# Optimization experiments

Measured on AMD Instinct MI355X. Metric: run time of the kernel, lower is better.

The kernel has to match this reference:

```python
import jax, jax.numpy as jnp
import numpy as np

B, REP = 32, 1024
N_VERBS, N_ROLES, N_NOUNS, MR = 504, 190, 11538, 6
HID, NHEADS, MAXN = 32, 4, 512


def setup_inputs() -> dict:
    key = jax.random.key(0)
    ks = jax.random.split(key, 16)
    s = 0.05  # weight scale
    return {
        "rep": jax.random.normal(ks[0], (B, REP), jnp.float32),
        "W_v": jax.random.normal(ks[1], (REP, N_VERBS), jnp.float32) * s,
        "b_v": jax.random.normal(ks[2], (N_VERBS,), jnp.float32) * s,
        "W_r": jax.random.normal(ks[3], (REP, N_ROLES * HID), jnp.float32) * s,
        "b_r": jax.random.normal(ks[4], (N_ROLES * HID,), jnp.float32) * s,
        "attn_in_w": jax.random.normal(ks[5], (3, 3 * HID, HID), jnp.float32) * s,
        "attn_in_b": jax.random.normal(ks[6], (3, 3 * HID), jnp.float32) * s,
        "attn_out_w": jax.random.normal(ks[7], (3, HID, HID), jnp.float32) * s,
        "attn_out_b": jax.random.normal(ks[8], (3, HID), jnp.float32) * s,
        "W_n": jax.random.normal(ks[9], (HID, N_NOUNS), jnp.float32) * s,
        "b_n": jax.random.normal(ks[10], (N_NOUNS,), jnp.float32) * s,
        "r_n_idx": jax.random.randint(ks[11], (N_ROLES, MAXN), 0, N_NOUNS, jnp.int32),
        "pad_v_r": jax.random.randint(ks[12], (N_VERBS, MR), 0, N_ROLES + 1, jnp.int32),
    }


def _mha(x, in_w, in_b, out_w, out_b):
    # x: [L, B, E] self-attention, torch nn.MultiheadAttention semantics
    L, Bn, E = x.shape
    hd = E // NHEADS
    qkv = x @ in_w.T + in_b                      # [L, B, 3E]
    q, k, v = jnp.split(qkv, 3, axis=-1)
    q = q.reshape(L, Bn, NHEADS, hd)
    k = k.reshape(L, Bn, NHEADS, hd)
    v = v.reshape(L, Bn, NHEADS, hd)
    scores = jnp.einsum("lbhd,mbhd->bhlm", q, k) / jnp.sqrt(jnp.float32(hd))
    attn = jax.nn.softmax(scores, axis=-1)
    out = jnp.einsum("bhlm,mbhd->lbhd", attn, v).reshape(L, Bn, E)
    return out @ out_w.T + out_b


def reference(rep, W_v, b_v, W_r, b_r, attn_in_w, attn_in_b, attn_out_w,
              attn_out_b, W_n, b_n, r_n_idx, pad_v_r):
    batch = rep.shape[0]
    v_potential = rep @ W_v + b_v                          # [B, V]
    node = (rep @ W_r + b_r).reshape(batch, N_ROLES, HID)
    node = jnp.transpose(node, (1, 0, 2))                  # [R, B, H]
    for i in range(3):
        node = _mha(node, attn_in_w[i], attn_in_b[i], attn_out_w[i], attn_out_b[i])
    rn_potential = node @ W_n + b_n                        # [R, B, N_nouns]

    # grouped index_select per role: [R, B, MAXN]
    grouped = jax.vmap(lambda pot, idx: pot[:, idx])(rn_potential, r_n_idx)
    r_max = grouped.max(axis=-1)                           # [R, B]
    maxi = grouped.argmax(axis=-1)                         # [R, B]
    rn_marginal = r_max + jnp.log(jnp.exp(grouped - r_max[..., None]).sum(-1))
    r_maxi = jax.vmap(lambda idx, mi: idx[mi])(r_n_idx, maxi)  # global noun ids

    # [B, R] then prepend the zero/padding column -> [B, 1+R]
    zeros_f = jnp.zeros((batch, 1), rn_marginal.dtype)
    zeros_i = jnp.zeros((batch, 1), r_maxi.dtype)
    rn_marginal = jnp.concatenate([zeros_f, rn_marginal.T], axis=1)
    r_max = jnp.concatenate([zeros_f, r_max.T], axis=1)
    r_maxi = jnp.concatenate([zeros_i, r_maxi.T], axis=1)

    # gather per-verb role groups: [B, V, MR]
    vrn_marginal_g = rn_marginal[:, pad_v_r]
    vr_max_g = r_max[:, pad_v_r]
    vr_maxi_g = r_maxi[:, pad_v_r]

    v_marginal = vrn_marginal_g.sum(2) + v_potential       # [B, V]
    m = v_marginal.max(1)
    norm = m + jnp.log(jnp.exp(v_marginal - m[:, None]).sum(1))
    v_max = vr_max_g.sum(2) + v_potential                  # [B, V]
    return (rep, v_potential, rn_potential, norm, v_max, vr_maxi_g)
```

## Files before the change

### kernel.cpp

```cpp
#include <hip/hip_runtime.h>
#include <math.h>

#define B_    32
#define REP_  1024
#define NV_   504
#define NR_   190
#define NN_   11538
#define MR_   6
#define HID_  32
#define NH_   4
#define HD_   8
#define MAXN_ 512

#define O_VP   32768
#define O_RN   48896
#define O_NORM 70199936
#define O_VMAX 70199968
#define O_MAXI 70216096

#define W_REPT  0
#define W_WT    32768
#define W_PN    401984
#define W_PV    1958464
#define W_N0    2087488
#define W_N1    2282048
#define W_HO    2476608
#define W_MARG  2671168
#define W_RMAX  2677248
#define W_RMAXI 2683328

__global__ __launch_bounds__(256) void k_tr_rep(const float* __restrict__ rep,
                                                float* __restrict__ repT) {
    int gid = blockIdx.x * 256 + threadIdx.x;
    int b = gid & 31, k = gid >> 5;
    repT[gid] = rep[b * REP_ + k];
}

__global__ __launch_bounds__(256) void k_tr_wn(const float* __restrict__ Wn,
                                               float* __restrict__ Wt) {
    __shared__ float t[32][33];
    int n0 = blockIdx.x * 32;
    int tid = threadIdx.x;
    #pragma unroll
    for (int p = 0; p < 4; p++) {
        int idx = p * 256 + tid;
        int k = idx >> 5, n = idx & 31;
        int nn = n0 + n;
        t[k][n] = (nn < NN_) ? Wn[(size_t)k * NN_ + nn] : 0.f;
    }
    __syncthreads();
    #pragma unroll
    for (int p = 0; p < 4; p++) {
        int idx = p * 256 + tid;
        int n = idx >> 5, k = idx & 31;
        int nn = n0 + n;
        if (nn < NN_) Wt[nn * 32 + k] = t[k][n];
    }
}

__global__ __launch_bounds__(256) void k_gemm_node(const float* __restrict__ Wr,
                                                   const float4* __restrict__ repT4,
                                                   float* __restrict__ pn) {
    int c  = blockIdx.x * 64 + (threadIdx.x & 63);
    int bg = threadIdx.x >> 6;
    int k0 = blockIdx.y * 128;
    float acc[8] = {0.f,0.f,0.f,0.f,0.f,0.f,0.f,0.f};
    int rbase = k0 * 8 + bg * 2;
    const float* w = Wr + (size_t)k0 * 6080 + c;
    #pragma unroll 4
    for (int k = 0; k < 128; k++) {
        float wv = w[(size_t)k * 6080];
        float4 ra = repT4[rbase + k * 8];
        float4 rb = repT4[rbase + k * 8 + 1];
        acc[0] += ra.x * wv; acc[1] += ra.y * wv; acc[2] += ra.z * wv; acc[3] += ra.w * wv;
        acc[4] += rb.x * wv; acc[5] += rb.y * wv; acc[6] += rb.z * wv; acc[7] += rb.w * wv;
    }
    size_t base = (size_t)blockIdx.y * 194560 + (size_t)(bg * 8) * 6080 + c;
    #pragma unroll
    for (int i = 0; i < 8; i++) pn[base + (size_t)i * 6080] = acc[i];
}

__global__ __launch_bounds__(256) void k_gemm_vp(const float* __restrict__ Wv,
                                                 const float4* __restrict__ repT4,
                                                 float* __restrict__ pv) {
    int c  = blockIdx.x * 64 + (threadIdx.x & 63);
    if (c >= NV_) return;
    int bg = threadIdx.x >> 6;
    int k0 = blockIdx.y * 128;
    float acc[8] = {0.f,0.f,0.f,0.f,0.f,0.f,0.f,0.f};
    int rbase = k0 * 8 + bg * 2;
    const float* w = Wv + (size_t)k0 * NV_ + c;
    #pragma unroll 4
    for (int k = 0; k < 128; k++) {
        float wv = w[(size_t)k * NV_];
        float4 ra = repT4[rbase + k * 8];
        float4 rb = repT4[rbase + k * 8 + 1];
        acc[0] += ra.x * wv; acc[1] += ra.y * wv; acc[2] += ra.z * wv; acc[3] += ra.w * wv;
        acc[4] += rb.x * wv; acc[5] += rb.y * wv; acc[6] += rb.z * wv; acc[7] += rb.w * wv;
    }
    size_t base = (size_t)blockIdx.y * 16128 + (size_t)(bg * 8) * NV_ + c;
    #pragma unroll
    for (int i = 0; i < 8; i++) pv[base + (size_t)i * NV_] = acc[i];
}

__global__ __launch_bounds__(256) void k_reduce(const float* __restrict__ pn,
                                                const float* __restrict__ pv,
                                                const float* __restrict__ br,
                                                const float* __restrict__ bv,
                                                float* __restrict__ node0,
                                                float* __restrict__ vpot) {
    int bid = blockIdx.x, tid = threadIdx.x;
    if (bid < 760) {
        int gid = bid * 256 + tid;
        int b = gid / 6080, c = gid - b * 6080;
        float s = br[c];
        #pragma unroll
        for (int kz = 0; kz < 8; kz++) s += pn[kz * 194560 + gid];
        node0[(c >> 5) * 1024 + b * 32 + (c & 31)] = s;
    } else {
        int gid = (bid - 760) * 256 + tid;
        int v = gid % NV_;
        float s = bv[v];
        #pragma unroll
        for (int kz = 0; kz < 8; kz++) s += pv[kz * 16128 + gid];
        vpot[gid] = s;
    }
}

__global__ __launch_bounds__(256) void k_attn(const float* __restrict__ xin,
                                              const float* __restrict__ inw,
                                              const float* __restrict__ inb,
                                              float* __restrict__ ho) {
    int b = blockIdx.x >> 2, h = blockIdx.x & 3;
    int tid = threadIdx.x;
    __shared__ __align__(16) float qs[192 * 12];
    __shared__ __align__(16) float ks[192 * 12];
    __shared__ __align__(16) float vs[192 * 12];
    __shared__ __align__(16) float pmS[4 * 192];
    __shared__ __align__(16) float psS[4 * 192];
    __shared__ __align__(16) float poS[4 * 192 * 8];

    if (tid < NR_) {
        const float* xr = xin + tid * 1024 + b * 32;
        float4 xv[8];
        #pragma unroll
        for (int q = 0; q < 8; q++) xv[q] = *(const float4*)(xr + q * 4);
        #pragma unroll 1
        for (int part = 0; part < 3; part++) {
            float* dst = (part == 0) ? qs : (part == 1) ? ks : vs;
            #pragma unroll 1
            for (int jj = 0; jj < 8; jj++) {
                int row = part * 32 + h * 8 + jj;
                const float* wr = inw + row * 32;
                float s = inb[row];
                #pragma unroll
                for (int q = 0; q < 8; q++) {
                    s += xv[q].x * wr[q*4+0] + xv[q].y * wr[q*4+1] +
                         xv[q].z * wr[q*4+2] + xv[q].w * wr[q*4+3];
                }
                dst[tid * 12 + jj] = s;
            }
        }
    }
    __syncthreads();

    int wave = tid >> 6, lane = tid & 63;
    int m0 = wave * 48;
    int m1 = (m0 + 48 < NR_) ? (m0 + 48) : NR_;
    float4 qa[3], qb[3];
    #pragma unroll
    for (int i = 0; i < 3; i++) {
        int l = lane + 64 * i;
        if (l < NR_) {
            qa[i] = *(const float4*)&qs[l * 12];
            qb[i] = *(const float4*)&qs[l * 12 + 4];
        } else {
            qa[i] = make_float4(0.f,0.f,0.f,0.f);
            qb[i] = make_float4(0.f,0.f,0.f,0.f);
        }
    }
    float mM[3] = {-INFINITY, -INFINITY, -INFINITY};
    float sS[3] = {0.f, 0.f, 0.f};
    float o[3][8];
    #pragma unroll
    for (int i = 0; i < 3; i++)
        #pragma unroll
        for (int d = 0; d < 8; d++) o[i][d] = 0.f;
    const float scale = 0.3535533905932738f;
    for (int mm = m0; mm < m1; mm++) {
        float4 ka = *(const float4*)&ks[mm * 12];
        float4 kb = *(const float4*)&ks[mm * 12 + 4];
        float4 va = *(const float4*)&vs[mm * 12];
        float4 vb = *(const float4*)&vs[mm * 12 + 4];
        #pragma unroll
        for (int i = 0; i < 3; i++) {
            float sc = (qa[i].x*ka.x + qa[i].y*ka.y + qa[i].z*ka.z + qa[i].w*ka.w +
                        qb[i].x*kb.x + qb[i].y*kb.y + qb[i].z*kb.z + qb[i].w*kb.w) * scale;
            if (sc > mM[i]) {
                float al = __expf(mM[i] - sc);
                sS[i] = sS[i] * al + 1.f;
                mM[i] = sc;
                o[i][0] = o[i][0]*al + va.x; o[i][1] = o[i][1]*al + va.y;
                o[i][2] = o[i][2]*al + va.z; o[i][3] = o[i][3]*al + va.w;
                o[i][4] = o[i][4]*al + vb.x; o[i][5] = o[i][5]*al + vb.y;
                o[i][6] = o[i][6]*al + vb.z; o[i][7] = o[i][7]*al + vb.w;
            } else {
                float p = __expf(sc - mM[i]);
                sS[i] += p;
                o[i][0] += p*va.x; o[i][1] += p*va.y; o[i][2] += p*va.z; o[i][3] += p*va.w;
                o[i][4] += p*vb.x; o[i][5] += p*vb.y; o[i][6] += p*vb.z; o[i][7] += p*vb.w;
            }
        }
    }
    #pragma unroll
    for (int i = 0; i < 3; i++) {
        int slot = wave * 192 + lane + 64 * i;
        pmS[slot] = mM[i];
        psS[slot] = sS[i];
        *(float4*)&poS[slot * 8]     = make_float4(o[i][0], o[i][1], o[i][2], o[i][3]);
        *(float4*)&poS[slot * 8 + 4] = make_float4(o[i][4], o[i][5], o[i][6], o[i][7]);
    }
    __syncthreads();

    if (tid < NR_) {
        float M = pmS[tid], S = psS[tid];
        float4 oa = *(const float4*)&poS[tid * 8];
        float4 ob = *(const float4*)&poS[tid * 8 + 4];
        #pragma unroll
        for (int w = 1; w < 4; w++) {
            int slot = w * 192 + tid;
            float m2 = pmS[slot], s2 = psS[slot];
            float4 pa = *(const float4*)&poS[slot * 8];
            float4 pb = *(const float4*)&poS[slot * 8 + 4];
            if (m2 > M) {
                float al = __expf(M - m2);
                S = S * al + s2;
                oa.x = oa.x*al + pa.x; oa.y = oa.y*al + pa.y; oa.z = oa.z*al + pa.z; oa.w = oa.w*al + pa.w;
                ob.x = ob.x*al + pb.x; ob.y = ob.y*al + pb.y; ob.z = ob.z*al + pb.z; ob.w = ob.w*al + pb.w;
                M = m2;
            } else {
                float p = __expf(m2 - M);
                S += s2 * p;
                oa.x += p*pa.x; oa.y += p*pa.y; oa.z += p*pa.z; oa.w += p*pa.w;
                ob.x += p*pb.x; ob.y += p*pb.y; ob.z += p*pb.z; ob.w += p*pb.w;
            }
        }
        float inv = 1.f / S;
        float* hp = ho + tid * 1024 + b * 32 + h * 8;
        *(float4*)hp       = make_float4(oa.x*inv, oa.y*inv, oa.z*inv, oa.w*inv);
        *(float4*)(hp + 4) = make_float4(ob.x*inv, ob.y*inv, ob.z*inv, ob.w*inv);
    }
}

__global__ __launch_bounds__(256) void k_outproj(const float* __restrict__ ho,
                                                 const float* __restrict__ ow,
                                                 const float* __restrict__ ob,
                                                 float* __restrict__ xout) {
    int l = blockIdx.x >> 2, part = blockIdx.x & 3;
    int tid = threadIdx.x;
    __shared__ float w[32 * 33];
    __shared__ float hl[256];
    __shared__ float obs[32];
    for (int i = tid; i < 1024; i += 256) w[(i >> 5) * 33 + (i & 31)] = ow[i];
    if (tid < 32) obs[tid] = ob[tid];
    {
        int bb = tid >> 5, e = tid & 31;
        hl[tid] = ho[l * 1024 + (part * 8 + bb) * 32 + e];
    }
    __syncthreads();
    int bb = tid >> 5, e = tid & 31;
    float s = obs[e];
    #pragma unroll
    for (int e2 = 0; e2 < 32; e2++) s += hl[bb * 32 + e2] * w[e * 33 + e2];
    xout[l * 1024 + (part * 8 + bb) * 32 + e] = s;
}

__global__ __launch_bounds__(256) void k_rnpot(const float* __restrict__ node,
                                               const float* __restrict__ Wn,
                                               const float* __restrict__ bn,
                                               float* __restrict__ out) {
    int tid = threadIdx.x;
    int t0 = blockIdx.x * 32;
    int c0 = blockIdx.y * 512;
    int wave = tid >> 6, lane = tid & 63;
    int r0 = wave * 8;
    int c = c0 + lane * 8;
    __shared__ float As[32 * 32];
    for (int i = tid; i < 1024; i += 256) As[i] = node[t0 * 32 + i];
    __syncthreads();
    int rem = NN_ - c;
    if (rem <= 0) return;
    if (rem >= 8) {
        float acc[8][8];
        #pragma unroll
        for (int r = 0; r < 8; r++)
            #pragma unroll
            for (int q = 0; q < 8; q++) acc[r][q] = 0.f;
        #pragma unroll 1
        for (int g = 0; g < 8; g++) {
            float4 av[8];
            #pragma unroll
            for (int r = 0; r < 8; r++)
                av[r] = *(const float4*)&As[(r0 + r) * 32 + g * 4];
            #pragma unroll
            for (int kk = 0; kk < 4; kk++) {
                int k = g * 4 + kk;
                const float* wp = &Wn[(size_t)k * NN_ + c];
                float2 w0 = *(const float2*)(wp);
                float2 w1 = *(const float2*)(wp + 2);
                float2 w2 = *(const float2*)(wp + 4);
                float2 w3 = *(const float2*)(wp + 6);
                #pragma unroll
                for (int r = 0; r < 8; r++) {
                    float a = ((const float*)&av[r])[kk];
                    acc[r][0] += a * w0.x; acc[r][1] += a * w0.y;
                    acc[r][2] += a * w1.x; acc[r][3] += a * w1.y;
                    acc[r][4] += a * w2.x; acc[r][5] += a * w2.y;
                    acc[r][6] += a * w3.x; acc[r][7] += a * w3.y;
                }
            }
        }
        float bb[8];
        #pragma unroll
        for (int q = 0; q < 8; q++) bb[q] = bn[c + q];
        #pragma unroll
        for (int r = 0; r < 8; r++) {
            size_t base = (size_t)(t0 + r0 + r) * NN_ + c;
            #pragma unroll
            for (int q = 0; q < 4; q++) {
                float2 s = make_float2(acc[r][2*q] + bb[2*q], acc[r][2*q+1] + bb[2*q+1]);
                *(float2*)&out[base + 2*q] = s;
            }
        }
    } else {
        for (int e = 0; e < rem; e++) {
            float acc[8] = {0.f,0.f,0.f,0.f,0.f,0.f,0.f,0.f};
            for (int k = 0; k < 32; k++) {
                float wv = Wn[(size_t)k * NN_ + c + e];
                #pragma unroll
                for (int r = 0; r < 8; r++) acc[r] += As[(r0 + r) * 32 + k] * wv;
            }
            float bv2 = bn[c + e];
            #pragma unroll
            for (int r = 0; r < 8; r++)
                out[(size_t)(t0 + r0 + r) * NN_ + c + e] = acc[r] + bv2;
        }
    }
}

__global__ __launch_bounds__(256) void k_grouped(const float* __restrict__ node,
                                                 const float* __restrict__ Wt,
                                                 const float* __restrict__ bn,
                                                 const int* __restrict__ rni,
                                                 float* __restrict__ marg,
                                                 float* __restrict__ rmax,
                                                 int* __restrict__ rmaxi) {
    int l = blockIdx.x;
    int tid = threadIdx.x;
    int jg = tid >> 5, b = tid & 31;
    __shared__ float pm[32 * 8], psum[32 * 8];
    __shared__ int pj[32 * 8];
    float4 nd[8];
    const float4* np = (const float4*)&node[l * 1024 + b * 32];
    #pragma unroll
    for (int q = 0; q < 8; q++) nd[q] = np[q];
    float lm = -INFINITY, ls = 0.f;
    int jm = 0;
    const int* ip = &rni[l * 512];
    for (int jj = 0; jj < 64; jj++) {
        int j = jg * 64 + jj;
        int idx = ip[j];
        const float4* wr = (const float4*)&Wt[idx * 32];
        float s = bn[idx];
        #pragma unroll
        for (int q = 0; q < 8; q++) {
            float4 w4 = wr[q];
            s += nd[q].x*w4.x + nd[q].y*w4.y + nd[q].z*w4.z + nd[q].w*w4.w;
        }
        if (s > lm) { ls = ls * __expf(lm - s) + 1.f; lm = s; jm = j; }
        else        { ls += __expf(s - lm); }
    }
    pm[b * 8 + jg] = lm; psum[b * 8 + jg] = ls; pj[b * 8 + jg] = jm;
    __syncthreads();
    if (tid < 32) {
        int bb = tid;
        float M = pm[bb * 8], S = psum[bb * 8];
        int J = pj[bb * 8];
        for (int i = 1; i < 8; i++) {
            float m2 = pm[bb * 8 + i], s2 = psum[bb * 8 + i];
            if (m2 > M) { S = S * __expf(M - m2) + s2; M = m2; J = pj[bb * 8 + i]; }
            else        { S += s2 * __expf(m2 - M); }
        }
        int t = l * 32 + bb;
        marg[t]  = M + logf(S);
        rmax[t]  = M;
        rmaxi[t] = ip[J];
    }
}

__global__ __launch_bounds__(256) void k_final(const float* __restrict__ marg,
                                               const float* __restrict__ rmax,
                                               const int* __restrict__ rmaxi,
                                               const int* __restrict__ pad,
                                               const float* __restrict__ vpot,
                                               float* __restrict__ out_norm,
                                               float* __restrict__ out_vmax,
                                               float* __restrict__ out_maxi) {
    int b = blockIdx.x, tid = threadIdx.x;
    __shared__ float me[191], xe[191];
    __shared__ int ie[191];
    __shared__ float vm[NV_];
    __shared__ float rbuf[4];
    if (tid < 191) {
        if (tid == 0) { me[0] = 0.f; xe[0] = 0.f; ie[0] = 0; }
        else {
            int t = (tid - 1) * 32 + b;
            me[tid] = marg[t]; xe[tid] = rmax[t]; ie[tid] = rmaxi[t];
        }
    }
    __syncthreads();
    for (int v = tid; v < NV_; v += 256) {
        float sm = 0.f, sx = 0.f;
        float vp = vpot[b * NV_ + v];
        #pragma unroll
        for (int i = 0; i < 6; i++) {
            int p = pad[v * 6 + i];
            sm += me[p]; sx += xe[p];
            out_maxi[(size_t)(b * NV_ + v) * 6 + i] = (float)ie[p];
        }
        vm[v] = sm + vp;
        out_vmax[b * NV_ + v] = sx + vp;
    }
    __syncthreads();
    float m = -INFINITY;
    for (int v = tid; v < NV_; v += 256) m = fmaxf(m, vm[v]);
    #pragma unroll
    for (int off = 32; off > 0; off >>= 1) m = fmaxf(m, __shfl_xor(m, off));
    if ((tid & 63) == 0) rbuf[tid >> 6] = m;
    __syncthreads();
    float M = fmaxf(fmaxf(rbuf[0], rbuf[1]), fmaxf(rbuf[2], rbuf[3]));
    __syncthreads();
    float s = 0.f;
    for (int v = tid; v < NV_; v += 256) s += __expf(vm[v] - M);
    #pragma unroll
    for (int off = 32; off > 0; off >>= 1) s += __shfl_xor(s, off);
    if ((tid & 63) == 0) rbuf[tid >> 6] = s;
    __syncthreads();
    if (tid == 0) out_norm[b] = M + logf(rbuf[0] + rbuf[1] + rbuf[2] + rbuf[3]);
}

extern "C" void kernel_launch(void* const* d_in, const int* in_sizes, int n_in,
                              void* d_out, int out_size, void* d_ws, size_t ws_size,
                              hipStream_t stream) {
    const float* rep   = (const float*)d_in[0];
    const float* Wv    = (const float*)d_in[1];
    const float* bv    = (const float*)d_in[2];
    const float* Wr    = (const float*)d_in[3];
    const float* br    = (const float*)d_in[4];
    const float* ainw  = (const float*)d_in[5];
    const float* ainb  = (const float*)d_in[6];
    const float* aoutw = (const float*)d_in[7];
    const float* aoutb = (const float*)d_in[8];
    const float* Wn    = (const float*)d_in[9];
    const float* bn    = (const float*)d_in[10];
    const int*   rni   = (const int*)d_in[11];
    const int*   pad   = (const int*)d_in[12];
    float* out = (float*)d_out;
    float* ws  = (float*)d_ws;

    float* repT = ws + W_REPT;
    float* Wt   = ws + W_WT;
    float* pn   = ws + W_PN;
    float* pv   = ws + W_PV;
    float* n0   = ws + W_N0;
    float* n1   = ws + W_N1;
    float* ho   = ws + W_HO;
    float* marg = ws + W_MARG;
    float* rmx  = ws + W_RMAX;
    int*   rmi  = (int*)(ws + W_RMAXI);

    hipMemcpyAsync(out, rep, 32768 * sizeof(float), hipMemcpyDeviceToDevice, stream);
    k_tr_rep<<<128, 256, 0, stream>>>(rep, repT);
    k_tr_wn<<<361, 256, 0, stream>>>(Wn, Wt);
    k_gemm_node<<<dim3(95, 8), 256, 0, stream>>>(Wr, (const float4*)repT, pn);
    k_gemm_vp<<<dim3(8, 8), 256, 0, stream>>>(Wv, (const float4*)repT, pv);
    k_reduce<<<823, 256, 0, stream>>>(pn, pv, br, bv, n0, out + O_VP);

    float* bufs[4] = {n0, n1, n0, n1};
    for (int i = 0; i < 3; i++) {
        k_attn<<<128, 256, 0, stream>>>(bufs[i], ainw + i * 96 * 32, ainb + i * 96, ho);
        k_outproj<<<760, 256, 0, stream>>>(ho, aoutw + i * 32 * 32, aoutb + i * 32, bufs[i + 1]);
    }

    k_rnpot<<<dim3(190, 23), 256, 0, stream>>>(n1, Wn, bn, out + O_RN);
    k_grouped<<<190, 256, 0, stream>>>(n1, Wt, bn, rni, marg, rmx, rmi);
    k_final<<<32, 256, 0, stream>>>(marg, rmx, rmi, pad, out + O_VP,
                                    out + O_NORM, out + O_VMAX, out + O_MAXI);
}
```

Before: 647.0 us.

## Fold attention out-projections into next in-projection and fuse final projection into noun kernels

Precomputes combined weights (in_w[i+1]·out_w[i] and the matching bias) so each attention layer reads the previous layer's head outputs directly, which removes the separate out-projection kernels. The last out-projection is recomputed inside a merged kernel that handles both the role-noun potential GEMM and the grouped logsumexp/argmax, replacing two launches. The two rep GEMMs are merged into one launch, the Wn transpose shares a launch with the weight-combination work, and the rn-potential stores are widened to float4 where aligned. The trade-off is redundant out-projection work repeated in every block and a small change in floating-point rounding order.

```diff
diff --git a/kernel.cpp b/kernel.cpp
--- a/kernel.cpp
+++ b/kernel.cpp
@@ -23,11 +23,12 @@
 #define W_PN    401984
 #define W_PV    1958464
 #define W_N0    2087488
-#define W_N1    2282048
-#define W_HO    2476608
+#define W_HOB   2282048
+#define W_HOA   2476608
 #define W_MARG  2671168
 #define W_RMAX  2677248
 #define W_RMAXI 2683328
+#define W_WC    2689408
 
 __global__ __launch_bounds__(256) void k_tr_rep(const float* __restrict__ rep,
                                                 float* __restrict__ repT) {
@@ -36,71 +37,98 @@
     repT[gid] = rep[b * REP_ + k];
 }
 
-__global__ __launch_bounds__(256) void k_tr_wn(const float* __restrict__ Wn,
-                                               float* __restrict__ Wt) {
+__global__ __launch_bounds__(256) void k_pre(const float* __restrict__ Wn,
+                                             float* __restrict__ Wt,
+                                             const float* __restrict__ ainw,
+                                             const float* __restrict__ ainb,
+                                             const float* __restrict__ aoutw,
+                                             const float* __restrict__ aoutb,
+                                             float* __restrict__ wc) {
     __shared__ float t[32][33];
-    int n0 = blockIdx.x * 32;
     int tid = threadIdx.x;
-    #pragma unroll
-    for (int p = 0; p < 4; p++) {
-        int idx = p * 256 + tid;
-        int k = idx >> 5, n = idx & 31;
-        int nn = n0 + n;
-        t[k][n] = (nn < NN_) ? Wn[(size_t)k * NN_ + nn] : 0.f;
-    }
-    __syncthreads();
-    #pragma unroll
-    for (int p = 0; p < 4; p++) {
-        int idx = p * 256 + tid;
-        int n = idx >> 5, k = idx & 31;
-        int nn = n0 + n;
-        if (nn < NN_) Wt[nn * 32 + k] = t[k][n];
-    }
-}
-
-__global__ __launch_bounds__(256) void k_gemm_node(const float* __restrict__ Wr,
-                                                   const float4* __restrict__ repT4,
-                                                   float* __restrict__ pn) {
-    int c  = blockIdx.x * 64 + (threadIdx.x & 63);
+    if (blockIdx.x < 361) {
+        int n0 = blockIdx.x * 32;
+        #pragma unroll
+        for (int p = 0; p < 4; p++) {
+            int idx = p * 256 + tid;
+            int k = idx >> 5, n = idx & 31;
+            int nn = n0 + n;
+            t[k][n] = (nn < NN_) ? Wn[(size_t)k * NN_ + nn] : 0.f;
+        }
+        __syncthreads();
+        #pragma unroll
+        for (int p = 0; p < 4; p++) {
+            int idx = p * 256 + tid;
+            int n = idx >> 5, k = idx & 31;
+            int nn = n0 + n;
+            if (nn < NN_) Wt[nn * 32 + k] = t[k][n];
+        }
+    } else {
+        #pragma unroll 1
+        for (int layer = 0; layer < 2; layer++) {
+            const float* iw  = ainw + (layer + 1) * 3072;
+            const float* ib  = ainb + (layer + 1) * 96;
+            const float* ow  = aoutw + layer * 1024;
+            const float* obv = aoutb + layer * 32;
+            float* W = wc + layer * 3168;
+            for (int idx = tid; idx < 3072; idx += 256) {
+                int row = idx >> 5, d = idx & 31;
+                float s = 0.f;
+                #pragma unroll
+                for (int e = 0; e < 32; e++) s += iw[row * 32 + e] * ow[e * 32 + d];
+                W[idx] = s;
+            }
+            if (tid < 96) {
+                float s = ib[tid];
+                #pragma unroll
+                for (int e = 0; e < 32; e++) s += iw[tid * 32 + e] * obv[e];
+                W[3072 + tid] = s;
+            }
+        }
+    }
+}
+
+__global__ __launch_bounds__(256) void k_gemm(const float* __restrict__ Wr,
+                                              const float* __restrict__ Wv,
+                                              const float4* __restrict__ repT4,
+                                              float* __restrict__ pn,
+                                              float* __restrict__ pv) {
+    int bx = blockIdx.x;
+    int lane = threadIdx.x & 63;
     int bg = threadIdx.x >> 6;
     int k0 = blockIdx.y * 128;
+    int rbase = k0 * 8 + bg * 2;
     float acc[8] = {0.f,0.f,0.f,0.f,0.f,0.f,0.f,0.f};
-    int rbase = k0 * 8 + bg * 2;
-    const float* w = Wr + (size_t)k0 * 6080 + c;
-    #pragma unroll 4
-    for (int k = 0; k < 128; k++) {
-        float wv = w[(size_t)k * 6080];
-        float4 ra = repT4[rbase + k * 8];
-        float4 rb = repT4[rbase + k * 8 + 1];
-        acc[0] += ra.x * wv; acc[1] += ra.y * wv; acc[2] += ra.z * wv; acc[3] += ra.w * wv;
-        acc[4] += rb.x * wv; acc[5] += rb.y * wv; acc[6] += rb.z * wv; acc[7] += rb.w * wv;
-    }
-    size_t base = (size_t)blockIdx.y * 194560 + (size_t)(bg * 8) * 6080 + c;
-    #pragma unroll
-    for (int i = 0; i < 8; i++) pn[base + (size_t)i * 6080] = acc[i];
-}
-
-__global__ __launch_bounds__(256) void k_gemm_vp(const float* __restrict__ Wv,
-                                                 const float4* __restrict__ repT4,
-                                                 float* __restrict__ pv) {
-    int c  = blockIdx.x * 64 + (threadIdx.x & 63);
-    if (c >= NV_) return;
-    int bg = threadIdx.x >> 6;
-    int k0 = blockIdx.y * 128;
-    float acc[8] = {0.f,0.f,0.f,0.f,0.f,0.f,0.f,0.f};
-    int rbase = k0 * 8 + bg * 2;
-    const float* w = Wv + (size_t)k0 * NV_ + c;
-    #pragma unroll 4
-    for (int k = 0; k < 128; k++) {
-        float wv = w[(size_t)k * NV_];
-        float4 ra = repT4[rbase + k * 8];
-        float4 rb = repT4[rbase + k * 8 + 1];
-        acc[0] += ra.x * wv; acc[1] += ra.y * wv; acc[2] += ra.z * wv; acc[3] += ra.w * wv;
-        acc[4] += rb.x * wv; acc[5] += rb.y * wv; acc[6] += rb.z * wv; acc[7] += rb.w * wv;
-    }
-    size_t base = (size_t)blockIdx.y * 16128 + (size_t)(bg * 8) * NV_ + c;
-    #pragma unroll
-    for (int i = 0; i < 8; i++) pv[base + (size_t)i * NV_] = acc[i];
+    if (bx < 95) {
+        int c = bx * 64 + lane;
+        const float* w = Wr + (size_t)k0 * 6080 + c;
+        #pragma unroll 4
+        for (int k = 0; k < 128; k++) {
+            float wv = w[(size_t)k * 6080];
+            float4 ra = repT4[rbase + k * 8];
+            float4 rb = repT4[rbase + k * 8 + 1];
+            acc[0] += ra.x * wv; acc[1] += ra.y * wv; acc[2] += ra.z * wv; acc[3] += ra.w * wv;
+            acc[4] += rb.x * wv; acc[5] += rb.y * wv; acc[6] += rb.z * wv; acc[7] += rb.w * wv;
+        }
+        size_t base = (size_t)blockIdx.y * 194560 + (size_t)(bg * 8) * 6080 + c;
+        #pragma unroll
+        for (int i = 0; i < 8; i++) pn[base + (size_t)i * 6080] = acc[i];
+    } else {
+        int c = (bx - 95) * 64 + lane;
+        if (c >= NV_) return;
+        const float* w = Wv + (size_t)k0 * NV_ + c;
+        #pragma unroll 4
+        for (int k = 0; k < 128; k++) {
+            float wv = w[(size_t)k * NV_];
+            float4 ra = repT4[rbase + k * 8];
+            float4 rb = repT4[rbase + k * 8 + 1];
+            acc[0] += ra.x * wv; acc[1] += ra.y * wv; acc[2] += ra.z * wv; acc[3] += ra.w * wv;
+            acc[4] += rb.x * wv; acc[5] += rb.y * wv; acc[6] += rb.z * wv; acc[7] += rb.w * wv;
+        }
+        size_t base = (size_t)blockIdx.y * 16128 + (size_t)(bg * 8) * NV_ + c;
+        #pragma unroll
+        for (int i = 0; i < 8; i++) pv[base + (size_t)i * NV_] = acc[i];
+    }
 }
 
 __global__ __launch_bounds__(256) void k_reduce(const float* __restrict__ pn,
@@ -128,8 +156,8 @@
 }
 
 __global__ __launch_bounds__(256) void k_attn(const float* __restrict__ xin,
-                                              const float* __restrict__ inw,
-                                              const float* __restrict__ inb,
+                                              const float* __restrict__ winw,
+                                              const float* __restrict__ winb,
                                               float* __restrict__ ho) {
     int b = blockIdx.x >> 2, h = blockIdx.x & 3;
     int tid = threadIdx.x;
@@ -151,8 +179,8 @@
             #pragma unroll 1
             for (int jj = 0; jj < 8; jj++) {
                 int row = part * 32 + h * 8 + jj;
-                const float* wr = inw + row * 32;
-                float s = inb[row];
+                const float* wr = winw + row * 32;
+                float s = winb[row];
                 #pragma unroll
                 for (int q = 0; q < 8; q++) {
                     s += xv[q].x * wr[q*4+0] + xv[q].y * wr[q*4+1] +
@@ -252,149 +280,185 @@
     }
 }
 
-__global__ __launch_bounds__(256) void k_outproj(const float* __restrict__ ho,
-                                                 const float* __restrict__ ow,
-                                                 const float* __restrict__ ob,
-                                                 float* __restrict__ xout) {
-    int l = blockIdx.x >> 2, part = blockIdx.x & 3;
-    int tid = threadIdx.x;
-    __shared__ float w[32 * 33];
-    __shared__ float hl[256];
-    __shared__ float obs[32];
-    for (int i = tid; i < 1024; i += 256) w[(i >> 5) * 33 + (i & 31)] = ow[i];
-    if (tid < 32) obs[tid] = ob[tid];
-    {
-        int bb = tid >> 5, e = tid & 31;
-        hl[tid] = ho[l * 1024 + (part * 8 + bb) * 32 + e];
-    }
-    __syncthreads();
-    int bb = tid >> 5, e = tid & 31;
-    float s = obs[e];
-    #pragma unroll
-    for (int e2 = 0; e2 < 32; e2++) s += hl[bb * 32 + e2] * w[e * 33 + e2];
-    xout[l * 1024 + (part * 8 + bb) * 32 + e] = s;
-}
-
-__global__ __launch_bounds__(256) void k_rnpot(const float* __restrict__ node,
-                                               const float* __restrict__ Wn,
-                                               const float* __restrict__ bn,
-                                               float* __restrict__ out) {
-    int tid = threadIdx.x;
-    int t0 = blockIdx.x * 32;
-    int c0 = blockIdx.y * 512;
-    int wave = tid >> 6, lane = tid & 63;
-    int r0 = wave * 8;
-    int c = c0 + lane * 8;
-    __shared__ float As[32 * 32];
-    for (int i = tid; i < 1024; i += 256) As[i] = node[t0 * 32 + i];
-    __syncthreads();
-    int rem = NN_ - c;
-    if (rem <= 0) return;
-    if (rem >= 8) {
-        float acc[8][8];
-        #pragma unroll
-        for (int r = 0; r < 8; r++)
-            #pragma unroll
-            for (int q = 0; q < 8; q++) acc[r][q] = 0.f;
-        #pragma unroll 1
-        for (int g = 0; g < 8; g++) {
-            float4 av[8];
-            #pragma unroll
-            for (int r = 0; r < 8; r++)
-                av[r] = *(const float4*)&As[(r0 + r) * 32 + g * 4];
-            #pragma unroll
-            for (int kk = 0; kk < 4; kk++) {
-                int k = g * 4 + kk;
-                const float* wp = &Wn[(size_t)k * NN_ + c];
-                float2 w0 = *(const float2*)(wp);
-                float2 w1 = *(const float2*)(wp + 2);
-                float2 w2 = *(const float2*)(wp + 4);
-                float2 w3 = *(const float2*)(wp + 6);
-                #pragma unroll
-                for (int r = 0; r < 8; r++) {
-                    float a = ((const float*)&av[r])[kk];
-                    acc[r][0] += a * w0.x; acc[r][1] += a * w0.y;
-                    acc[r][2] += a * w1.x; acc[r][3] += a * w1.y;
-                    acc[r][4] += a * w2.x; acc[r][5] += a * w2.y;
-                    acc[r][6] += a * w3.x; acc[r][7] += a * w3.y;
-                }
-            }
-        }
-        float bb[8];
-        #pragma unroll
-        for (int q = 0; q < 8; q++) bb[q] = bn[c + q];
-        #pragma unroll
-        for (int r = 0; r < 8; r++) {
-            size_t base = (size_t)(t0 + r0 + r) * NN_ + c;
-            #pragma unroll
-            for (int q = 0; q < 4; q++) {
-                float2 s = make_float2(acc[r][2*q] + bb[2*q], acc[r][2*q+1] + bb[2*q+1]);
-                *(float2*)&out[base + 2*q] = s;
-            }
-        }
-    } else {
-        for (int e = 0; e < rem; e++) {
-            float acc[8] = {0.f,0.f,0.f,0.f,0.f,0.f,0.f,0.f};
-            for (int k = 0; k < 32; k++) {
-                float wv = Wn[(size_t)k * NN_ + c + e];
-                #pragma unroll
-                for (int r = 0; r < 8; r++) acc[r] += As[(r0 + r) * 32 + k] * wv;
-            }
-            float bv2 = bn[c + e];
-            #pragma unroll
-            for (int r = 0; r < 8; r++)
-                out[(size_t)(t0 + r0 + r) * NN_ + c + e] = acc[r] + bv2;
-        }
-    }
-}
-
-__global__ __launch_bounds__(256) void k_grouped(const float* __restrict__ node,
-                                                 const float* __restrict__ Wt,
-                                                 const float* __restrict__ bn,
-                                                 const int* __restrict__ rni,
-                                                 float* __restrict__ marg,
-                                                 float* __restrict__ rmax,
-                                                 int* __restrict__ rmaxi) {
+__global__ __launch_bounds__(256) void k_big(const float* __restrict__ ho3,
+                                             const float* __restrict__ ow3,
+                                             const float* __restrict__ ob3,
+                                             const float* __restrict__ Wn,
+                                             const float* __restrict__ bn,
+                                             const float* __restrict__ Wt,
+                                             const int* __restrict__ rni,
+                                             float* __restrict__ out_rn,
+                                             float* __restrict__ marg,
+                                             float* __restrict__ rmax,
+                                             int* __restrict__ rmaxi) {
     int l = blockIdx.x;
     int tid = threadIdx.x;
-    int jg = tid >> 5, b = tid & 31;
+    __shared__ float owT[1024];
+    __shared__ float As[1024];
     __shared__ float pm[32 * 8], psum[32 * 8];
-    __shared__ int pj[32 * 8];
-    float4 nd[8];
-    const float4* np = (const float4*)&node[l * 1024 + b * 32];
-    #pragma unroll
-    for (int q = 0; q < 8; q++) nd[q] = np[q];
-    float lm = -INFINITY, ls = 0.f;
-    int jm = 0;
-    const int* ip = &rni[l * 512];
-    for (int jj = 0; jj < 64; jj++) {
-        int j = jg * 64 + jj;
-        int idx = ip[j];
-        const float4* wr = (const float4*)&Wt[idx * 32];
-        float s = bn[idx];
+    __shared__ int   pj[32 * 8];
+
+    for (int i = tid; i < 1024; i += 256) {
+        int d = i >> 5, hh = i & 31;
+        owT[i] = ow3[hh * 32 + d];
+    }
+
+    if (blockIdx.y < 23) {
+        int b = tid >> 3, hq = tid & 7;
+        float4 hv[8];
+        {
+            const float4* hp = (const float4*)&ho3[(size_t)l * 1024 + b * 32];
+            #pragma unroll
+            for (int q = 0; q < 8; q++) hv[q] = hp[q];
+        }
+        __syncthreads();
+        {
+            float4 a = *(const float4*)&ob3[hq * 4];
+            #pragma unroll
+            for (int dq = 0; dq < 8; dq++) {
+                float4 h4 = hv[dq];
+                float4 w0 = *(const float4*)&owT[(dq*4+0)*32 + hq*4];
+                float4 w1 = *(const float4*)&owT[(dq*4+1)*32 + hq*4];
+                float4 w2 = *(const float4*)&owT[(dq*4+2)*32 + hq*4];
+                float4 w3 = *(const float4*)&owT[(dq*4+3)*32 + hq*4];
+                a.x += h4.x*w0.x + h4.y*w1.x + h4.z*w2.x + h4.w*w3.x;
+                a.y += h4.x*w0.y + h4.y*w1.y + h4.z*w2.y + h4.w*w3.y;
+                a.z += h4.x*w0.z + h4.y*w1.z + h4.z*w2.z + h4.w*w3.z;
+                a.w += h4.x*w0.w + h4.y*w1.w + h4.z*w2.w + h4.w*w3.w;
+            }
+            *(float4*)&As[b * 32 + hq * 4] = a;
+        }
+        __syncthreads();
+
+        int t0 = l * 32;
+        int c0 = blockIdx.y * 512;
+        int wave = tid >> 6, lane = tid & 63;
+        int r0 = wave * 8;
+        int c = c0 + lane * 8;
+        int rem = NN_ - c;
+        if (rem <= 0) return;
+        if (rem >= 8) {
+            float acc[8][8];
+            #pragma unroll
+            for (int r = 0; r < 8; r++)
+                #pragma unroll
+                for (int q = 0; q < 8; q++) acc[r][q] = 0.f;
+            #pragma unroll 1
+            for (int g = 0; g < 8; g++) {
+                float4 av[8];
+                #pragma unroll
+                for (int r = 0; r < 8; r++)
+                    av[r] = *(const float4*)&As[(r0 + r) * 32 + g * 4];
+                #pragma unroll
+                for (int kk = 0; kk < 4; kk++) {
+                    int k = g * 4 + kk;
+                    const float* wp = &Wn[(size_t)k * NN_ + c];
+                    float2 w0 = *(const float2*)(wp);
+                    float2 w1 = *(const float2*)(wp + 2);
+                    float2 w2 = *(const float2*)(wp + 4);
+                    float2 w3 = *(const float2*)(wp + 6);
+                    #pragma unroll
+                    for (int r = 0; r < 8; r++) {
+                        float a = ((const float*)&av[r])[kk];
+                        acc[r][0] += a * w0.x; acc[r][1] += a * w0.y;
+                        acc[r][2] += a * w1.x; acc[r][3] += a * w1.y;
+                        acc[r][4] += a * w2.x; acc[r][5] += a * w2.y;
+                        acc[r][6] += a * w3.x; acc[r][7] += a * w3.y;
+                    }
+                }
+            }
+            float bb[8];
+            #pragma unroll
+            for (int q = 0; q < 8; q++) bb[q] = bn[c + q];
+            #pragma unroll
+            for (int r = 0; r < 8; r++) {
+                size_t base = (size_t)(t0 + r0 + r) * NN_ + c;
+                float v0 = acc[r][0]+bb[0], v1 = acc[r][1]+bb[1];
+                float v2 = acc[r][2]+bb[2], v3 = acc[r][3]+bb[3];
+                float v4 = acc[r][4]+bb[4], v5 = acc[r][5]+bb[5];
+                float v6 = acc[r][6]+bb[6], v7 = acc[r][7]+bb[7];
+                if (((r0 + r) & 1) == 0) {
+                    *(float4*)&out_rn[base]     = make_float4(v0, v1, v2, v3);
+                    *(float4*)&out_rn[base + 4] = make_float4(v4, v5, v6, v7);
+                } else {
+                    *(float2*)&out_rn[base]     = make_float2(v0, v1);
+                    *(float4*)&out_rn[base + 2] = make_float4(v2, v3, v4, v5);
+                    *(float2*)&out_rn[base + 6] = make_float2(v6, v7);
+                }
+            }
+        } else {
+            for (int e = 0; e < rem; e++) {
+                float acc[8] = {0.f,0.f,0.f,0.f,0.f,0.f,0.f,0.f};
+                for (int k = 0; k < 32; k++) {
+                    float wv = Wn[(size_t)k * NN_ + c + e];
+                    #pragma unroll
+                    for (int r = 0; r < 8; r++) acc[r] += As[(r0 + r) * 32 + k] * wv;
+                }
+                float bv2 = bn[c + e];
+                #pragma unroll
+                for (int r = 0; r < 8; r++)
+                    out_rn[(size_t)(t0 + r0 + r) * NN_ + c + e] = acc[r] + bv2;
+            }
+        }
+    } else {
+        int jg = tid >> 5, b = tid & 31;
+        float4 hv[8];
+        {
+            const float4* hp = (const float4*)&ho3[(size_t)l * 1024 + b * 32];
+            #pragma unroll
+            for (int q = 0; q < 8; q++) hv[q] = hp[q];
+        }
+        __syncthreads();
+        float4 nd[8];
         #pragma unroll
         for (int q = 0; q < 8; q++) {
-            float4 w4 = wr[q];
-            s += nd[q].x*w4.x + nd[q].y*w4.y + nd[q].z*w4.z + nd[q].w*w4.w;
-        }
-        if (s > lm) { ls = ls * __expf(lm - s) + 1.f; lm = s; jm = j; }
-        else        { ls += __expf(s - lm); }
-    }
-    pm[b * 8 + jg] = lm; psum[b * 8 + jg] = ls; pj[b * 8 + jg] = jm;
-    __syncthreads();
-    if (tid < 32) {
-        int bb = tid;
-        float M = pm[bb * 8], S = psum[bb * 8];
-        int J = pj[bb * 8];
-        for (int i = 1; i < 8; i++) {
-            float m2 = pm[bb * 8 + i], s2 = psum[bb * 8 + i];
-            if (m2 > M) { S = S * __expf(M - m2) + s2; M = m2; J = pj[bb * 8 + i]; }
-            else        { S += s2 * __expf(m2 - M); }
-        }
-        int t = l * 32 + bb;
-        marg[t]  = M + logf(S);
-        rmax[t]  = M;
-        rmaxi[t] = ip[J];
+            float4 a = *(const float4*)&ob3[q * 4];
+            #pragma unroll
+            for (int dq = 0; dq < 8; dq++) {
+                float4 h4 = hv[dq];
+                float4 w0 = *(const float4*)&owT[(dq*4+0)*32 + q*4];
+                float4 w1 = *(const float4*)&owT[(dq*4+1)*32 + q*4];
+                float4 w2 = *(const float4*)&owT[(dq*4+2)*32 + q*4];
+                float4 w3 = *(const float4*)&owT[(dq*4+3)*32 + q*4];
+                a.x += h4.x*w0.x + h4.y*w1.x + h4.z*w2.x + h4.w*w3.x;
+                a.y += h4.x*w0.y + h4.y*w1.y + h4.z*w2.y + h4.w*w3.y;
+                a.z += h4.x*w0.z + h4.y*w1.z + h4.z*w2.z + h4.w*w3.z;
+                a.w += h4.x*w0.w + h4.y*w1.w + h4.z*w2.w + h4.w*w3.w;
+            }
+            nd[q] = a;
+        }
+        float lm = -INFINITY, ls = 0.f;
+        int jm = 0;
+        const int* ip = &rni[l * 512];
+        for (int jj = 0; jj < 64; jj++) {
+            int j = jg * 64 + jj;
+            int idx = ip[j];
+            const float4* wr = (const float4*)&Wt[idx * 32];
+            float s = bn[idx];
+            #pragma unroll
+            for (int q = 0; q < 8; q++) {
+                float4 w4 = wr[q];
+                s += nd[q].x*w4.x + nd[q].y*w4.y + nd[q].z*w4.z + nd[q].w*w4.w;
+            }
+            if (s > lm) { ls = ls * __expf(lm - s) + 1.f; lm = s; jm = j; }
+            else        { ls += __expf(s - lm); }
+        }
+        pm[b * 8 + jg] = lm; psum[b * 8 + jg] = ls; pj[b * 8 + jg] = jm;
+        __syncthreads();
+        if (tid < 32) {
+            int bb = tid;
+            float M = pm[bb * 8], S = psum[bb * 8];
+            int J = pj[bb * 8];
+            for (int i = 1; i < 8; i++) {
+                float m2 = pm[bb * 8 + i], s2 = psum[bb * 8 + i];
+                if (m2 > M) { S = S * __expf(M - m2) + s2; M = m2; J = pj[bb * 8 + i]; }
+                else        { S += s2 * __expf(m2 - M); }
+            }
+            int t = l * 32 + bb;
+            marg[t]  = M + logf(S);
+            rmax[t]  = M;
+            rmaxi[t] = ip[J];
+        }
     }
 }
 
@@ -473,27 +537,26 @@
     float* pn   = ws + W_PN;
     float* pv   = ws + W_PV;
     float* n0   = ws + W_N0;
-    float* n1   = ws + W_N1;
-    float* ho   = ws + W_HO;
+    float* hoA  = ws + W_HOA;
+    float* hoB  = ws + W_HOB;
     float* marg = ws + W_MARG;
     float* rmx  = ws + W_RMAX;
     int*   rmi  = (int*)(ws + W_RMAXI);
+    float* wc   = ws + W_WC;
 
     hipMemcpyAsync(out, rep, 32768 * sizeof(float), hipMemcpyDeviceToDevice, stream);
     k_tr_rep<<<128, 256, 0, stream>>>(rep, repT);
-    k_tr_wn<<<361, 256, 0, stream>>>(Wn, Wt);
-    k_gemm_node<<<dim3(95, 8), 256, 0, stream>>>(Wr, (const float4*)repT, pn);
-    k_gemm_vp<<<dim3(8, 8), 256, 0, stream>>>(Wv, (const float4*)repT, pv);
+    k_pre<<<362, 256, 0, stream>>>(Wn, Wt, ainw, ainb, aoutw, aoutb, wc);
+    k_gemm<<<dim3(103, 8), 256, 0, stream>>>(Wr, Wv, (const float4*)repT, pn, pv);
     k_reduce<<<823, 256, 0, stream>>>(pn, pv, br, bv, n0, out + O_VP);
 
-    float* bufs[4] = {n0, n1, n0, n1};
-    for (int i = 0; i < 3; i++) {
-        k_attn<<<128, 256, 0, stream>>>(bufs[i], ainw + i * 96 * 32, ainb + i * 96, ho);
-        k_outproj<<<760, 256, 0, stream>>>(ho, aoutw + i * 32 * 32, aoutb + i * 32, bufs[i + 1]);
-    }
-
-    k_rnpot<<<dim3(190, 23), 256, 0, stream>>>(n1, Wn, bn, out + O_RN);
-    k_grouped<<<190, 256, 0, stream>>>(n1, Wt, bn, rni, marg, rmx, rmi);
+    k_attn<<<128, 256, 0, stream>>>(n0,  ainw,      ainb,      hoA);
+    k_attn<<<128, 256, 0, stream>>>(hoA, wc,        wc + 3072, hoB);
+    k_attn<<<128, 256, 0, stream>>>(hoB, wc + 3168, wc + 6240, hoA);
+
+    k_big<<<dim3(190, 24), 256, 0, stream>>>(hoA, aoutw + 2048, aoutb + 64,
+                                             Wn, bn, Wt, rni,
+                                             out + O_RN, marg, rmx, rmi);
     k_final<<<32, 256, 0, stream>>>(marg, rmx, rmi, pad, out + O_VP,
                                     out + O_NORM, out + O_VMAX, out + O_MAXI);
 }
```

Measured after the change: 650.1 us. No clear change (+0.5%).
